# Optimization experiments

Hardware: AMD Instinct MI355X
Metric: run time of the kernel (lower is better)

## Reference

```python
import jax, jax.numpy as jnp
import numpy as np
from jax import lax


def _sobel_kernel(k=3):
    r = np.linspace(-(k // 2), k // 2, k)
    x, y = np.meshgrid(r, r)
    den = x ** 2 + y ** 2
    den[:, k // 2] = 1.0
    return (x / den).astype(np.float32)  # [[-.5,0,.5],[-1,0,1],[-.5,0,.5]]


def _thin_kernels():
    # 8 directional kernels: +1 at center, -1 at the neighbor at angle k*45 deg
    # (counterclockwise), exactly what the cv2 rotation in the torch code produces.
    offsets = [(0, 1), (-1, 1), (-1, 0), (-1, -1), (0, -1), (1, -1), (1, 0), (1, 1)]
    ker = np.zeros((8, 1, 3, 3), dtype=np.float32)
    for i, (dy, dx) in enumerate(offsets):
        ker[i, 0, 1, 1] = 1.0
        ker[i, 0, 1 + dy, 1 + dx] = -1.0
    return ker


def _conv(x, w):
    # cross-correlation, SAME padding, NCHW/OIHW -- matches torch Conv2d
    return lax.conv_general_dilated(x, w, window_strides=(1, 1), padding='SAME',
                                    dimension_numbers=('NCHW', 'OIHW', 'NCHW'))


def setup_inputs() -> dict:
    key = jax.random.key(0)
    img = jax.random.normal(key, (16, 1, 1024, 1024), dtype=jnp.float32)
    sob = _sobel_kernel(3)
    return {
        'img': img,
        'w_x': jnp.asarray(sob).reshape(1, 1, 3, 3),
        'w_y': jnp.asarray(sob.T).reshape(1, 1, 3, 3),
        'w_dir': jnp.asarray(_thin_kernels()),
        'threshold': jnp.float32(0.5),
    }


def reference(img, w_x, w_y, w_dir, threshold):
    grad_x = _conv(img, w_x)
    grad_y = _conv(img, w_y)
    grad_mag = jnp.sqrt(grad_x ** 2 + grad_y ** 2)  # [B,1,H,W]

    ori = jnp.arctan(grad_y / grad_x) * (360.0 / np.pi) + 180.0
    ori = jnp.round(ori / 45.0) * 45.0
    pos_idx = (ori / 45.0) % 8.0  # integer-valued float in {0..7}

    directional = _conv(grad_mag, w_dir)  # [B,8,H,W]

    # per-pixel direction d = pos_idx mod 4; pixel survives NMS iff both the
    # d and d+4 directional differences (center minus neighbor) are > 0
    idx4 = jnp.clip((pos_idx % 4.0).astype(jnp.int32), 0, 3)  # [B,1,H,W]
    dir_min = jnp.minimum(directional[:, :4], directional[:, 4:])  # [B,4,H,W]
    keep = jnp.take_along_axis(dir_min > 0.0, idx4, axis=1)  # [B,1,H,W] bool
    thin_edges = jnp.where(keep, grad_mag, 0.0)

    out = thin_edges - threshold
    out_forw = (out > 0.0).astype(out.dtype)  # heaviside(out, 0)
    out_bckw = jax.nn.sigmoid(out)
    return out_bckw + lax.stop_gradient(out_forw - out_bckw)
```

## Files before the change

kernel.cpp:

```cpp
#include <hip/hip_runtime.h>
#include <math.h>


constexpr int W = 1024, H = 1024;
constexpr int TX = 128, TY = 16;
constexpr int GH = TY + 2, GSTR = 132;

__device__ __forceinline__ void sobel_pair(float a00, float a01, float a02,
                                           float a10, float a12,
                                           float a20, float a21, float a22,
                                           float& gxv, float& gyv) {
  float t1 = 0.5f * (a02 - a00);
  float t2 = t1 - a10;
  float t3 = t2 + a12;
  float t4 = t3 - 0.5f * a20;
  gxv = t4 + 0.5f * a22;
  float p1 = 0.5f * a00 + a01;
  float p2 = p1 + 0.5f * a02;
  float u3 = 0.5f * a20 - p2;
  float u4 = u3 + a21;
  gyv = u4 + 0.5f * a22;
}

__device__ __forceinline__ float gld(const float* __restrict__ im, int r, int c) {
  const bool ok = ((unsigned)r < 1024u) && ((unsigned)c < 1024u);
  const int rc = min(max(r, 0), 1023);
  const int cc = min(max(c, 0), 1023);
  const float v = im[rc * W + cc];
  return ok ? v : 0.0f;
}

__device__ __forceinline__ float decide(float gxv, float gyv, float sc,
                                        float s0a, float s0b, float s1a, float s1b,
                                        float s2a, float s2b, float s3a, float s3b,
                                        float thr, float thr2) {
#pragma clang fp contract(off)
  const float T1 = 0.19891236737965801f, D1 = 5.0e-5f;
  const float T2 = 0.66817863791929898f, D2 = 7.0e-5f;
  const float T3 = 1.49660576266548901f, D3 = 1.5e-4f;
  const float T4 = 5.02733949212584810f, D4 = 1.2e-3f;

  const float av = fabsf(gyv), bv = fabsf(gxv);
  const float c1 = fmaf(-T1, bv, av);
  const float c2 = fmaf(-T2, bv, av);
  const float c3 = fmaf(-T3, bv, av);
  const float c4 = fmaf(-T4, bv, av);
  const bool nearb = (fabsf(c1) < D1 * bv) || (fabsf(c2) < D2 * bv) ||
                     (fabsf(c3) < D3 * bv) || (fabsf(c4) < D4 * bv);

  const unsigned sgn = (__float_as_uint(gyv) ^ __float_as_uint(gxv)) >> 31;

  const float m0 = fmaxf(fmaxf(s0a, s0b), thr2);
  const float m1 = fmaxf(fmaxf(s1a, s1b), thr2);
  const float m2 = fmaxf(fmaxf(s2a, s2b), thr2);
  const float m3 = fmaxf(fmaxf(s3a, s3b), thr2);
  float m;
  if (c1 < 0.0f)      m = m0;
  else if (c2 < 0.0f) m = sgn ? m3 : m1;
  else if (c3 < 0.0f) m = m2;
  else if (c4 < 0.0f) m = sgn ? m1 : m3;
  else                m = m0;

  const float scl = sc * 0.999998f;
  const bool raw  = (sc  > m);
  const bool sure = (scl > m);

  const bool need = nearb || (raw != sure);
  float res = sure ? 1.0f : 0.0f;

  if (__builtin_expect(__any((int)need), 0)) {
    const float C = (float)(360.0 / M_PI);
    float r  = gyv / gxv;
    float t  = atanf(r);
    float u  = t * C;
    float v2 = u + 180.0f;
    float w  = v2 / 45.0f;
    int   kk = (int)rintf(w);
    int   dd = kk & 3;
    float sn1e = (dd == 0) ? s0a : (dd == 1) ? s1a : (dd == 2) ? s2a : s3a;
    float sn2e = (dd == 0) ? s0b : (dd == 1) ? s1b : (dd == 2) ? s2b : s3b;
    float gmc = sqrtf(sc), n1 = sqrtf(sn1e), n2 = sqrtf(sn2e);
    bool keep = (gmc - n1 > 0.0f) && (gmc - n2 > 0.0f) && (gmc - thr > 0.0f);
    float slow = keep ? 1.0f : 0.0f;
    res = need ? slow : res;
  }
  return res;
}

__global__ __launch_bounds__(256)
void canny_kernel(const float* __restrict__ img, const float* __restrict__ thrp,
                  float* __restrict__ out) {
#pragma clang fp contract(off)
  __shared__ __align__(16) float s_sq[GH][GSTR];

  const int b   = blockIdx.z;
  const int bx0 = blockIdx.x * TX;
  const int by0 = blockIdx.y * TY;
  const float* im = img + (size_t)b * (W * H);
  float* ob       = out + (size_t)b * (W * H);
  const int tid = threadIdx.x;
  const bool edge = (bx0 == 0) || (bx0 + TX == W) || (by0 == 0) || (by0 + TY == H);

  const int c  = tid & 127;
  const int tz = tid >> 7;
  const int k0 = 9 * tz;

  float iA0, iB0, iC0, iA1, iB1, iC1, iA2, iB2, iC2, iA3, iB3, iC3;
  float iA4, iB4, iC4, iA5, iB5, iC5, iA6, iB6, iC6, iA7, iB7, iC7;
  float iA8, iB8, iC8, iA9, iB9, iC9, iA10, iB10, iC10;
  if (!edge) {
    const float* p = im + (size_t)(by0 + k0 - 2) * W + (bx0 + c - 1);
    iA0  = p[0 * W + 0];  iB0  = p[0 * W + 1];  iC0  = p[0 * W + 2];
    iA1  = p[1 * W + 0];  iB1  = p[1 * W + 1];  iC1  = p[1 * W + 2];
    iA2  = p[2 * W + 0];  iB2  = p[2 * W + 1];  iC2  = p[2 * W + 2];
    iA3  = p[3 * W + 0];  iB3  = p[3 * W + 1];  iC3  = p[3 * W + 2];
    iA4  = p[4 * W + 0];  iB4  = p[4 * W + 1];  iC4  = p[4 * W + 2];
    iA5  = p[5 * W + 0];  iB5  = p[5 * W + 1];  iC5  = p[5 * W + 2];
    iA6  = p[6 * W + 0];  iB6  = p[6 * W + 1];  iC6  = p[6 * W + 2];
    iA7  = p[7 * W + 0];  iB7  = p[7 * W + 1];  iC7  = p[7 * W + 2];
    iA8  = p[8 * W + 0];  iB8  = p[8 * W + 1];  iC8  = p[8 * W + 2];
    iA9  = p[9 * W + 0];  iB9  = p[9 * W + 1];  iC9  = p[9 * W + 2];
    iA10 = p[10 * W + 0]; iB10 = p[10 * W + 1]; iC10 = p[10 * W + 2];
  } else {
    const int r0 = by0 + k0 - 2;
    const int cb = bx0 + c;
    iA0  = gld(im, r0 + 0, cb - 1);  iB0  = gld(im, r0 + 0, cb);  iC0  = gld(im, r0 + 0, cb + 1);
    iA1  = gld(im, r0 + 1, cb - 1);  iB1  = gld(im, r0 + 1, cb);  iC1  = gld(im, r0 + 1, cb + 1);
    iA2  = gld(im, r0 + 2, cb - 1);  iB2  = gld(im, r0 + 2, cb);  iC2  = gld(im, r0 + 2, cb + 1);
    iA3  = gld(im, r0 + 3, cb - 1);  iB3  = gld(im, r0 + 3, cb);  iC3  = gld(im, r0 + 3, cb + 1);
    iA4  = gld(im, r0 + 4, cb - 1);  iB4  = gld(im, r0 + 4, cb);  iC4  = gld(im, r0 + 4, cb + 1);
    iA5  = gld(im, r0 + 5, cb - 1);  iB5  = gld(im, r0 + 5, cb);  iC5  = gld(im, r0 + 5, cb + 1);
    iA6  = gld(im, r0 + 6, cb - 1);  iB6  = gld(im, r0 + 6, cb);  iC6  = gld(im, r0 + 6, cb + 1);
    iA7  = gld(im, r0 + 7, cb - 1);  iB7  = gld(im, r0 + 7, cb);  iC7  = gld(im, r0 + 7, cb + 1);
    iA8  = gld(im, r0 + 8, cb - 1);  iB8  = gld(im, r0 + 8, cb);  iC8  = gld(im, r0 + 8, cb + 1);
    iA9  = gld(im, r0 + 9, cb - 1);  iB9  = gld(im, r0 + 9, cb);  iC9  = gld(im, r0 + 9, cb + 1);
    iA10 = gld(im, r0 + 10, cb - 1); iB10 = gld(im, r0 + 10, cb); iC10 = gld(im, r0 + 10, cb + 1);
  }

  const int rowim0 = by0 + k0 - 1;

  float t0, t1, t2, t3, t4, t5, t6, t7, t8;
  float sx0, sx1, sx2, sx3, sx4, sx5, sx6, sx7, sx8;
  float sy0, sy1, sy2, sy3, sy4, sy5, sy6, sy7, sy8;

#define GM_ROW(J, A0, B0, C0, A1, C1, A2, B2, C2, T, SX, SY)                   \
  {                                                                            \
    float gxv, gyv;                                                            \
    sobel_pair(A0, B0, C0, A1, C1, A2, B2, C2, gxv, gyv);                      \
    float sq = gxv * gxv + gyv * gyv;                                          \
    if (edge) { if ((unsigned)(rowim0 + J) >= 1024u) sq = 0.0f; }              \
    s_sq[k0 + J][c + 1] = sq;                                                  \
    T = sq; SX = gxv; SY = gyv;                                                \
  }

  GM_ROW(0, iA0, iB0, iC0, iA1, iC1, iA2, iB2, iC2, t0, sx0, sy0)
  GM_ROW(1, iA1, iB1, iC1, iA2, iC2, iA3, iB3, iC3, t1, sx1, sy1)
  GM_ROW(2, iA2, iB2, iC2, iA3, iC3, iA4, iB4, iC4, t2, sx2, sy2)
  GM_ROW(3, iA3, iB3, iC3, iA4, iC4, iA5, iB5, iC5, t3, sx3, sy3)
  GM_ROW(4, iA4, iB4, iC4, iA5, iC5, iA6, iB6, iC6, t4, sx4, sy4)
  GM_ROW(5, iA5, iB5, iC5, iA6, iC6, iA7, iB7, iC7, t5, sx5, sy5)
  GM_ROW(6, iA6, iB6, iC6, iA7, iC7, iA8, iB8, iC8, t6, sx6, sy6)
  GM_ROW(7, iA7, iB7, iC7, iA8, iC8, iA9, iB9, iC9, t7, sx7, sy7)
  GM_ROW(8, iA8, iB8, iC8, iA9, iC9, iA10, iB10, iC10, t8, sx8, sy8)
#undef GM_ROW

  if (tid < 36) {
    int rr = tid >> 1;
    int r  = rr - 1;
    int cc = (tid & 1) ? 128 : -1;
    int hr = by0 - 2 + rr;
    int hc = bx0 + cc;
    float gxv, gyv;
    sobel_pair(gld(im, hr, hc - 1),     gld(im, hr, hc),     gld(im, hr, hc + 1),
               gld(im, hr + 1, hc - 1),                      gld(im, hr + 1, hc + 1),
               gld(im, hr + 2, hc - 1), gld(im, hr + 2, hc), gld(im, hr + 2, hc + 1),
               gxv, gyv);
    float sq = gxv * gxv + gyv * gyv;
    if (!((unsigned)(by0 + r) < 1024u && (unsigned)(bx0 + cc) < 1024u)) sq = 0.0f;
    s_sq[rr][cc + 1] = sq;
  }
  __syncthreads();

  {
    const float thr  = *thrp;
    const float thr2 = thr * thr;
    const int gb = 8 * tz;
    const float L0 = s_sq[gb + 0][c], R0 = s_sq[gb + 0][c + 2];
    const float L1 = s_sq[gb + 1][c], R1 = s_sq[gb + 1][c + 2];
    const float L2 = s_sq[gb + 2][c], R2 = s_sq[gb + 2][c + 2];
    const float L3 = s_sq[gb + 3][c], R3 = s_sq[gb + 3][c + 2];
    const float L4 = s_sq[gb + 4][c], R4 = s_sq[gb + 4][c + 2];
    const float L5 = s_sq[gb + 5][c], R5 = s_sq[gb + 5][c + 2];
    const float L6 = s_sq[gb + 6][c], R6 = s_sq[gb + 6][c + 2];
    const float L7 = s_sq[gb + 7][c], R7 = s_sq[gb + 7][c + 2];
    const float L8 = s_sq[gb + 8][c], R8 = s_sq[gb + 8][c + 2];
    const float L9 = s_sq[gb + 9][c], R9 = s_sq[gb + 9][c + 2];

    float q0, q1, q2, q3, q4, q5, q6, q7, q8, q9;
    float X0, X1, X2, X3, X4, X5, X6, X7;
    float Y0, Y1, Y2, Y3, Y4, Y5, Y6, Y7;
    if (tz == 0) {
      q0 = t0; q1 = t1; q2 = t2; q3 = t3; q4 = t4;
      q5 = t5; q6 = t6; q7 = t7; q8 = t8;
      q9 = s_sq[9][c + 1];
      X0 = sx1; X1 = sx2; X2 = sx3; X3 = sx4; X4 = sx5; X5 = sx6; X6 = sx7; X7 = sx8;
      Y0 = sy1; Y1 = sy2; Y2 = sy3; Y3 = sy4; Y4 = sy5; Y5 = sy6; Y6 = sy7; Y7 = sy8;
    } else {
      q0 = s_sq[8][c + 1];
      q1 = t0; q2 = t1; q3 = t2; q4 = t3; q5 = t4;
      q6 = t5; q7 = t6; q8 = t7; q9 = t8;
      X0 = sx0; X1 = sx1; X2 = sx2; X3 = sx3; X4 = sx4; X5 = sx5; X6 = sx6; X7 = sx7;
      Y0 = sy0; Y1 = sy1; Y2 = sy2; Y3 = sy3; Y4 = sy4; Y5 = sy5; Y6 = sy7 - (sy7 - sy6) - (sy6 - sy6);
      Y6 = sy6; Y7 = sy7;
    }

    float* orow = ob + (size_t)(by0 + gb) * W + bx0 + c;

    orow[0 * W] = decide(X0, Y0, q1, R1, L1, R0, L2, q0, q2, L0, R2, thr, thr2);
    orow[1 * W] = decide(X1, Y1, q2, R2, L2, R1, L3, q1, q3, L1, R3, thr, thr2);
    orow[2 * W] = decide(X2, Y2, q3, R3, L3, R2, L4, q2, q4, L2, R4, thr, thr2);
    orow[3 * W] = decide(X3, Y3, q4, R4, L4, R3, L5, q3, q5, L3, R5, thr, thr2);
    orow[4 * W] = decide(X4, Y4, q5, R5, L5, R4, L6, q4, q6, L4, R6, thr, thr2);
    orow[5 * W] = decide(X5, Y5, q6, R6, L6, R5, L7, q5, q7, L5, R7, thr, thr2);
    orow[6 * W] = decide(X6, Y6, q7, R7, L7, R6, L8, q6, q8, L6, R8, thr, thr2);
    orow[7 * W] = decide(X7, Y7, q8, R8, L8, R7, L9, q7, q9, L7, R9, thr, thr2);
  }
}

extern "C" void kernel_launch(void* const* d_in, const int* in_sizes, int n_in,
                              void* d_out, int out_size, void* d_ws, size_t ws_size,
                              hipStream_t stream) {
  const float* img = (const float*)d_in[0];
  const float* thr = (const float*)d_in[4];
  float* out = (float*)d_out;
  const int batch = in_sizes[0] / (W * H);

  dim3 grid(W / TX, H / TY, batch);
  canny_kernel<<<grid, dim3(256), 0, stream>>>(img, thr, out);
}
```

Before: 42.86 us.

## Pack two rows per thread into float2 vectors for packed-math Sobel and NMS

Halves the block to 128 threads. Each thread now processes two rows eight apart as float2 vectors, so the Sobel, magnitude and direction-threshold arithmetic can use packed FP32 instructions (v_pk_fma_f32). The near-boundary test is rewritten as a min over FMA-based margins to cut compares, and the per-pixel tail stays scalar. The aim is to cut the VALU instruction count, at the cost of more registers per thread, fewer waves per block, and some FMA contraction that may change rounding slightly.

```diff
diff --git a/kernel.cpp b/kernel.cpp
--- a/kernel.cpp
+++ b/kernel.cpp
@@ -6,20 +6,27 @@
 constexpr int TX = 128, TY = 16;
 constexpr int GH = TY + 2, GSTR = 132;
 
-__device__ __forceinline__ void sobel_pair(float a00, float a01, float a02,
-                                           float a10, float a12,
-                                           float a20, float a21, float a22,
-                                           float& gxv, float& gyv) {
-  float t1 = 0.5f * (a02 - a00);
-  float t2 = t1 - a10;
-  float t3 = t2 + a12;
-  float t4 = t3 - 0.5f * a20;
-  gxv = t4 + 0.5f * a22;
-  float p1 = 0.5f * a00 + a01;
-  float p2 = p1 + 0.5f * a02;
-  float u3 = 0.5f * a20 - p2;
-  float u4 = u3 + a21;
-  gyv = u4 + 0.5f * a22;
+typedef float v2f __attribute__((ext_vector_type(2)));
+
+__device__ __forceinline__ v2f splat2(float a) { v2f v; v.x = a; v.y = a; return v; }
+__device__ __forceinline__ v2f fma2(float a, v2f b, v2f c) {
+  return __builtin_elementwise_fma(splat2(a), b, c);
+}
+
+__device__ __forceinline__ void sobel_pair2(v2f a00, v2f a01, v2f a02,
+                                            v2f a10, v2f a12,
+                                            v2f a20, v2f a21, v2f a22,
+                                            v2f& gxv, v2f& gyv) {
+  v2f t1 = splat2(0.5f) * (a02 - a00);
+  v2f t2 = t1 - a10;
+  v2f t3 = t2 + a12;
+  v2f t4 = fma2(-0.5f, a20, t3);
+  gxv = fma2(0.5f, a22, t4);
+  v2f p1 = fma2(0.5f, a00, a01);
+  v2f p2 = fma2(0.5f, a02, p1);
+  v2f u3 = fma2(0.5f, a20, -p2);
+  v2f u4 = u3 + a21;
+  gyv = fma2(0.5f, a22, u4);
 }
 
 __device__ __forceinline__ float gld(const float* __restrict__ im, int r, int c) {
@@ -30,26 +37,15 @@
   return ok ? v : 0.0f;
 }
 
-__device__ __forceinline__ float decide(float gxv, float gyv, float sc,
-                                        float s0a, float s0b, float s1a, float s1b,
-                                        float s2a, float s2b, float s3a, float s3b,
-                                        float thr, float thr2) {
+__device__ __forceinline__ float decide_tail(
+    float gxv, float gyv, float sc,
+    float c1, float c2, float c3, float c4, float emin, float scl,
+    float s0a, float s0b, float s1a, float s1b,
+    float s2a, float s2b, float s3a, float s3b,
+    float thr, float thr2) {
 #pragma clang fp contract(off)
-  const float T1 = 0.19891236737965801f, D1 = 5.0e-5f;
-  const float T2 = 0.66817863791929898f, D2 = 7.0e-5f;
-  const float T3 = 1.49660576266548901f, D3 = 1.5e-4f;
-  const float T4 = 5.02733949212584810f, D4 = 1.2e-3f;
-
-  const float av = fabsf(gyv), bv = fabsf(gxv);
-  const float c1 = fmaf(-T1, bv, av);
-  const float c2 = fmaf(-T2, bv, av);
-  const float c3 = fmaf(-T3, bv, av);
-  const float c4 = fmaf(-T4, bv, av);
-  const bool nearb = (fabsf(c1) < D1 * bv) || (fabsf(c2) < D2 * bv) ||
-                     (fabsf(c3) < D3 * bv) || (fabsf(c4) < D4 * bv);
-
+  const bool nearb = emin < 0.0f;
   const unsigned sgn = (__float_as_uint(gyv) ^ __float_as_uint(gxv)) >> 31;
-
   const float m0 = fmaxf(fmaxf(s0a, s0b), thr2);
   const float m1 = fmaxf(fmaxf(s1a, s1b), thr2);
   const float m2 = fmaxf(fmaxf(s2a, s2b), thr2);
@@ -60,14 +56,10 @@
   else if (c3 < 0.0f) m = m2;
   else if (c4 < 0.0f) m = sgn ? m1 : m3;
   else                m = m0;
-
-  const float scl = sc * 0.999998f;
   const bool raw  = (sc  > m);
   const bool sure = (scl > m);
-
   const bool need = nearb || (raw != sure);
   float res = sure ? 1.0f : 0.0f;
-
   if (__builtin_expect(__any((int)need), 0)) {
     const float C = (float)(360.0 / M_PI);
     float r  = gyv / gxv;
@@ -87,7 +79,41 @@
   return res;
 }
 
-__global__ __launch_bounds__(256)
+__device__ __forceinline__ v2f decide2(v2f gxv, v2f gyv, v2f sc,
+                                       v2f s0a, v2f s0b, v2f s1a, v2f s1b,
+                                       v2f s2a, v2f s2b, v2f s3a, v2f s3b,
+                                       float thr, float thr2) {
+#pragma clang fp contract(off)
+  const float T1 = 0.19891236737965801f, D1 = 5.0e-5f;
+  const float T2 = 0.66817863791929898f, D2 = 7.0e-5f;
+  const float T3 = 1.49660576266548901f, D3 = 1.5e-4f;
+  const float T4 = 5.02733949212584810f, D4 = 1.2e-3f;
+
+  const v2f av = __builtin_elementwise_abs(gyv);
+  const v2f bv = __builtin_elementwise_abs(gxv);
+  const v2f c1 = fma2(-T1, bv, av);
+  const v2f c2 = fma2(-T2, bv, av);
+  const v2f c3 = fma2(-T3, bv, av);
+  const v2f c4 = fma2(-T4, bv, av);
+  const v2f e1 = fma2(-D1, bv, __builtin_elementwise_abs(c1));
+  const v2f e2 = fma2(-D2, bv, __builtin_elementwise_abs(c2));
+  const v2f e3 = fma2(-D3, bv, __builtin_elementwise_abs(c3));
+  const v2f e4 = fma2(-D4, bv, __builtin_elementwise_abs(c4));
+  const v2f emin = __builtin_elementwise_min(__builtin_elementwise_min(e1, e2),
+                                             __builtin_elementwise_min(e3, e4));
+  const v2f scl = sc * splat2(0.999998f);
+
+  v2f res;
+  res.x = decide_tail(gxv.x, gyv.x, sc.x, c1.x, c2.x, c3.x, c4.x, emin.x, scl.x,
+                      s0a.x, s0b.x, s1a.x, s1b.x, s2a.x, s2b.x, s3a.x, s3b.x,
+                      thr, thr2);
+  res.y = decide_tail(gxv.y, gyv.y, sc.y, c1.y, c2.y, c3.y, c4.y, emin.y, scl.y,
+                      s0a.y, s0b.y, s1a.y, s1b.y, s2a.y, s2b.y, s3a.y, s3b.y,
+                      thr, thr2);
+  return res;
+}
+
+__global__ __launch_bounds__(128)
 void canny_kernel(const float* __restrict__ img, const float* __restrict__ thrp,
                   float* __restrict__ out) {
 #pragma clang fp contract(off)
@@ -99,70 +125,87 @@
   const float* im = img + (size_t)b * (W * H);
   float* ob       = out + (size_t)b * (W * H);
   const int tid = threadIdx.x;
+  const int c   = tid;
   const bool edge = (bx0 == 0) || (bx0 + TX == W) || (by0 == 0) || (by0 + TY == H);
 
-  const int c  = tid & 127;
-  const int tz = tid >> 7;
-  const int k0 = 9 * tz;
-
-  float iA0, iB0, iC0, iA1, iB1, iC1, iA2, iB2, iC2, iA3, iB3, iC3;
-  float iA4, iB4, iC4, iA5, iB5, iC5, iA6, iB6, iC6, iA7, iB7, iC7;
-  float iA8, iB8, iC8, iA9, iB9, iC9, iA10, iB10, iC10;
+  const float thr  = *thrp;
+  const float thr2 = thr * thr;
+
+  v2f PA0, PA1, PA2, PA3, PA4, PA5, PA6, PA7, PA8, PA9, PA10, PA11;
+  v2f PB0, PB1, PB2, PB3, PB4, PB5, PB6, PB7, PB8, PB9, PB10, PB11;
+  v2f PC0, PC1, PC2, PC3, PC4, PC5, PC6, PC7, PC8, PC9, PC10, PC11;
   if (!edge) {
-    const float* p = im + (size_t)(by0 + k0 - 2) * W + (bx0 + c - 1);
-    iA0  = p[0 * W + 0];  iB0  = p[0 * W + 1];  iC0  = p[0 * W + 2];
-    iA1  = p[1 * W + 0];  iB1  = p[1 * W + 1];  iC1  = p[1 * W + 2];
-    iA2  = p[2 * W + 0];  iB2  = p[2 * W + 1];  iC2  = p[2 * W + 2];
-    iA3  = p[3 * W + 0];  iB3  = p[3 * W + 1];  iC3  = p[3 * W + 2];
-    iA4  = p[4 * W + 0];  iB4  = p[4 * W + 1];  iC4  = p[4 * W + 2];
-    iA5  = p[5 * W + 0];  iB5  = p[5 * W + 1];  iC5  = p[5 * W + 2];
-    iA6  = p[6 * W + 0];  iB6  = p[6 * W + 1];  iC6  = p[6 * W + 2];
-    iA7  = p[7 * W + 0];  iB7  = p[7 * W + 1];  iC7  = p[7 * W + 2];
-    iA8  = p[8 * W + 0];  iB8  = p[8 * W + 1];  iC8  = p[8 * W + 2];
-    iA9  = p[9 * W + 0];  iB9  = p[9 * W + 1];  iC9  = p[9 * W + 2];
-    iA10 = p[10 * W + 0]; iB10 = p[10 * W + 1]; iC10 = p[10 * W + 2];
+    const float* p = im + (size_t)(by0 - 2) * W + (bx0 + c - 1);
+#define MKP(J)                                                                 \
+    PA##J = (v2f){p[(J) * W + 0], p[((J) + 8) * W + 0]};                       \
+    PB##J = (v2f){p[(J) * W + 1], p[((J) + 8) * W + 1]};                       \
+    PC##J = (v2f){p[(J) * W + 2], p[((J) + 8) * W + 2]};
+    MKP(0) MKP(1) MKP(2) MKP(3) MKP(4) MKP(5)
+    MKP(6) MKP(7) MKP(8) MKP(9) MKP(10) MKP(11)
+#undef MKP
   } else {
-    const int r0 = by0 + k0 - 2;
     const int cb = bx0 + c;
-    iA0  = gld(im, r0 + 0, cb - 1);  iB0  = gld(im, r0 + 0, cb);  iC0  = gld(im, r0 + 0, cb + 1);
-    iA1  = gld(im, r0 + 1, cb - 1);  iB1  = gld(im, r0 + 1, cb);  iC1  = gld(im, r0 + 1, cb + 1);
-    iA2  = gld(im, r0 + 2, cb - 1);  iB2  = gld(im, r0 + 2, cb);  iC2  = gld(im, r0 + 2, cb + 1);
-    iA3  = gld(im, r0 + 3, cb - 1);  iB3  = gld(im, r0 + 3, cb);  iC3  = gld(im, r0 + 3, cb + 1);
-    iA4  = gld(im, r0 + 4, cb - 1);  iB4  = gld(im, r0 + 4, cb);  iC4  = gld(im, r0 + 4, cb + 1);
-    iA5  = gld(im, r0 + 5, cb - 1);  iB5  = gld(im, r0 + 5, cb);  iC5  = gld(im, r0 + 5, cb + 1);
-    iA6  = gld(im, r0 + 6, cb - 1);  iB6  = gld(im, r0 + 6, cb);  iC6  = gld(im, r0 + 6, cb + 1);
-    iA7  = gld(im, r0 + 7, cb - 1);  iB7  = gld(im, r0 + 7, cb);  iC7  = gld(im, r0 + 7, cb + 1);
-    iA8  = gld(im, r0 + 8, cb - 1);  iB8  = gld(im, r0 + 8, cb);  iC8  = gld(im, r0 + 8, cb + 1);
-    iA9  = gld(im, r0 + 9, cb - 1);  iB9  = gld(im, r0 + 9, cb);  iC9  = gld(im, r0 + 9, cb + 1);
-    iA10 = gld(im, r0 + 10, cb - 1); iB10 = gld(im, r0 + 10, cb); iC10 = gld(im, r0 + 10, cb + 1);
-  }
-
-  const int rowim0 = by0 + k0 - 1;
-
-  float t0, t1, t2, t3, t4, t5, t6, t7, t8;
-  float sx0, sx1, sx2, sx3, sx4, sx5, sx6, sx7, sx8;
-  float sy0, sy1, sy2, sy3, sy4, sy5, sy6, sy7, sy8;
-
-#define GM_ROW(J, A0, B0, C0, A1, C1, A2, B2, C2, T, SX, SY)                   \
+    const int ccm1 = max(cb - 1, 0);
+    const int ccp1 = min(cb + 1, 1023);
+    const bool okL = (cb - 1) >= 0;
+    const bool okR = (cb + 1) <= 1023;
+    const int r0 = by0 - 2;
+    float vA0, vA1, vA2, vA3, vA4, vA5, vA6, vA7, vA8, vA9;
+    float vA10, vA11, vA12, vA13, vA14, vA15, vA16, vA17, vA18, vA19;
+    float vB0, vB1, vB2, vB3, vB4, vB5, vB6, vB7, vB8, vB9;
+    float vB10, vB11, vB12, vB13, vB14, vB15, vB16, vB17, vB18, vB19;
+    float vC0, vC1, vC2, vC3, vC4, vC5, vC6, vC7, vC8, vC9;
+    float vC10, vC11, vC12, vC13, vC14, vC15, vC16, vC17, vC18, vC19;
+#define LOADROW(J)                                                             \
+    {                                                                          \
+      const int rj = r0 + (J);                                                 \
+      const bool rOK = (unsigned)rj < 1024u;                 \
+      const int rc = min(max(rj, 0), 1023);                                    \
+      const float* rp = im + (size_t)rc * W;                                   \
+      const float va = rp[ccm1], vb = rp[cb], vc = rp[ccp1];                   \
+      vA##J = (rOK && okL) ? va : 0.0f;                                        \
+      vB##J = rOK ? vb : 0.0f;                                                 \
+      vC##J = (rOK && okR) ? vc : 0.0f;                                        \
+    }
+    LOADROW(0) LOADROW(1) LOADROW(2) LOADROW(3) LOADROW(4)
+    LOADROW(5) LOADROW(6) LOADROW(7) LOADROW(8) LOADROW(9)
+    LOADROW(10) LOADROW(11) LOADROW(12) LOADROW(13) LOADROW(14)
+    LOADROW(15) LOADROW(16) LOADROW(17) LOADROW(18) LOADROW(19)
+#undef LOADROW
+#define MKP(J, J8)                                                             \
+    PA##J = (v2f){vA##J, vA##J8};                                              \
+    PB##J = (v2f){vB##J, vB##J8};                                              \
+    PC##J = (v2f){vC##J, vC##J8};
+    MKP(0, 8) MKP(1, 9) MKP(2, 10) MKP(3, 11) MKP(4, 12) MKP(5, 13)
+    MKP(6, 14) MKP(7, 15) MKP(8, 16) MKP(9, 17) MKP(10, 18) MKP(11, 19)
+#undef MKP
+  }
+
+  v2f sq0, sq1, sq2v, sq3, sq4, sq5, sq6, sq7, sq8, sq9;
+  v2f ga0, ga1, ga2, ga3, ga4, ga5, ga6, ga7, ga8, ga9;
+  v2f gb0, gb1, gb2, gb3, gb4, gb5, gb6, gb7, gb8, gb9;
+#define GM_PAIR(J, A0, B0, C0, A1, C1, A2, B2, C2, SQ, GX, GY)                 \
   {                                                                            \
-    float gxv, gyv;                                                            \
-    sobel_pair(A0, B0, C0, A1, C1, A2, B2, C2, gxv, gyv);                      \
-    float sq = gxv * gxv + gyv * gyv;                                          \
-    if (edge) { if ((unsigned)(rowim0 + J) >= 1024u) sq = 0.0f; }              \
-    s_sq[k0 + J][c + 1] = sq;                                                  \
-    T = sq; SX = gxv; SY = gyv;                                                \
-  }
-
-  GM_ROW(0, iA0, iB0, iC0, iA1, iC1, iA2, iB2, iC2, t0, sx0, sy0)
-  GM_ROW(1, iA1, iB1, iC1, iA2, iC2, iA3, iB3, iC3, t1, sx1, sy1)
-  GM_ROW(2, iA2, iB2, iC2, iA3, iC3, iA4, iB4, iC4, t2, sx2, sy2)
-  GM_ROW(3, iA3, iB3, iC3, iA4, iC4, iA5, iB5, iC5, t3, sx3, sy3)
-  GM_ROW(4, iA4, iB4, iC4, iA5, iC5, iA6, iB6, iC6, t4, sx4, sy4)
-  GM_ROW(5, iA5, iB5, iC5, iA6, iC6, iA7, iB7, iC7, t5, sx5, sy5)
-  GM_ROW(6, iA6, iB6, iC6, iA7, iC7, iA8, iB8, iC8, t6, sx6, sy6)
-  GM_ROW(7, iA7, iB7, iC7, iA8, iC8, iA9, iB9, iC9, t7, sx7, sy7)
-  GM_ROW(8, iA8, iB8, iC8, iA9, iC9, iA10, iB10, iC10, t8, sx8, sy8)
-#undef GM_ROW
+    sobel_pair2(A0, B0, C0, A1, C1, A2, B2, C2, GX, GY);                       \
+    SQ = GX * GX + GY * GY;                                                    \
+    if (edge) {                                                                \
+      if ((unsigned)(by0 + (J) - 1) >= 1024u) SQ.x = 0.0f;                     \
+      if ((unsigned)(by0 + (J) + 7) >= 1024u) SQ.y = 0.0f;                     \
+    }                                                                          \
+    s_sq[(J)][c + 1] = SQ.x;                                                   \
+    s_sq[(J) + 8][c + 1] = SQ.y;                                               \
+  }
+  GM_PAIR(0, PA0, PB0, PC0, PA1, PC1, PA2, PB2, PC2, sq0, ga0, gb0)
+  GM_PAIR(1, PA1, PB1, PC1, PA2, PC2, PA3, PB3, PC3, sq1, ga1, gb1)
+  GM_PAIR(2, PA2, PB2, PC2, PA3, PC3, PA4, PB4, PC4, sq2v, ga2, gb2)
+  GM_PAIR(3, PA3, PB3, PC3, PA4, PC4, PA5, PB5, PC5, sq3, ga3, gb3)
+  GM_PAIR(4, PA4, PB4, PC4, PA5, PC5, PA6, PB6, PC6, sq4, ga4, gb4)
+  GM_PAIR(5, PA5, PB5, PC5, PA6, PC6, PA7, PB7, PC7, sq5, ga5, gb5)
+  GM_PAIR(6, PA6, PB6, PC6, PA7, PC7, PA8, PB8, PC8, sq6, ga6, gb6)
+  GM_PAIR(7, PA7, PB7, PC7, PA8, PC8, PA9, PB9, PC9, sq7, ga7, gb7)
+  GM_PAIR(8, PA8, PB8, PC8, PA9, PC9, PA10, PB10, PC10, sq8, ga8, gb8)
+  GM_PAIR(9, PA9, PB9, PC9, PA10, PC10, PA11, PB11, PC11, sq9, ga9, gb9)
+#undef GM_PAIR
 
   if (tid < 36) {
     int rr = tid >> 1;
@@ -171,10 +214,21 @@
     int hr = by0 - 2 + rr;
     int hc = bx0 + cc;
     float gxv, gyv;
-    sobel_pair(gld(im, hr, hc - 1),     gld(im, hr, hc),     gld(im, hr, hc + 1),
-               gld(im, hr + 1, hc - 1),                      gld(im, hr + 1, hc + 1),
-               gld(im, hr + 2, hc - 1), gld(im, hr + 2, hc), gld(im, hr + 2, hc + 1),
-               gxv, gyv);
+    {
+      float a00 = gld(im, hr, hc - 1),     a01 = gld(im, hr, hc),     a02 = gld(im, hr, hc + 1);
+      float a10 = gld(im, hr + 1, hc - 1),                            a12 = gld(im, hr + 1, hc + 1);
+      float a20 = gld(im, hr + 2, hc - 1), a21 = gld(im, hr + 2, hc), a22 = gld(im, hr + 2, hc + 1);
+      float t1 = 0.5f * (a02 - a00);
+      float t2 = t1 - a10;
+      float t3 = t2 + a12;
+      float t4 = fmaf(-0.5f, a20, t3);
+      gxv = fmaf(0.5f, a22, t4);
+      float p1 = fmaf(0.5f, a00, a01);
+      float p2 = fmaf(0.5f, a02, p1);
+      float u3 = fmaf(0.5f, a20, -p2);
+      float u4 = u3 + a21;
+      gyv = fmaf(0.5f, a22, u4);
+    }
     float sq = gxv * gxv + gyv * gyv;
     if (!((unsigned)(by0 + r) < 1024u && (unsigned)(bx0 + cc) < 1024u)) sq = 0.0f;
     s_sq[rr][cc + 1] = sq;
@@ -182,48 +236,35 @@
   __syncthreads();
 
   {
-    const float thr  = *thrp;
-    const float thr2 = thr * thr;
-    const int gb = 8 * tz;
-    const float L0 = s_sq[gb + 0][c], R0 = s_sq[gb + 0][c + 2];
-    const float L1 = s_sq[gb + 1][c], R1 = s_sq[gb + 1][c + 2];
-    const float L2 = s_sq[gb + 2][c], R2 = s_sq[gb + 2][c + 2];
-    const float L3 = s_sq[gb + 3][c], R3 = s_sq[gb + 3][c + 2];
-    const float L4 = s_sq[gb + 4][c], R4 = s_sq[gb + 4][c + 2];
-    const float L5 = s_sq[gb + 5][c], R5 = s_sq[gb + 5][c + 2];
-    const float L6 = s_sq[gb + 6][c], R6 = s_sq[gb + 6][c + 2];
-    const float L7 = s_sq[gb + 7][c], R7 = s_sq[gb + 7][c + 2];
-    const float L8 = s_sq[gb + 8][c], R8 = s_sq[gb + 8][c + 2];
-    const float L9 = s_sq[gb + 9][c], R9 = s_sq[gb + 9][c + 2];
-
-    float q0, q1, q2, q3, q4, q5, q6, q7, q8, q9;
-    float X0, X1, X2, X3, X4, X5, X6, X7;
-    float Y0, Y1, Y2, Y3, Y4, Y5, Y6, Y7;
-    if (tz == 0) {
-      q0 = t0; q1 = t1; q2 = t2; q3 = t3; q4 = t4;
-      q5 = t5; q6 = t6; q7 = t7; q8 = t8;
-      q9 = s_sq[9][c + 1];
-      X0 = sx1; X1 = sx2; X2 = sx3; X3 = sx4; X4 = sx5; X5 = sx6; X6 = sx7; X7 = sx8;
-      Y0 = sy1; Y1 = sy2; Y2 = sy3; Y3 = sy4; Y4 = sy5; Y5 = sy6; Y6 = sy7; Y7 = sy8;
-    } else {
-      q0 = s_sq[8][c + 1];
-      q1 = t0; q2 = t1; q3 = t2; q4 = t3; q5 = t4;
-      q6 = t5; q7 = t6; q8 = t7; q9 = t8;
-      X0 = sx0; X1 = sx1; X2 = sx2; X3 = sx3; X4 = sx4; X5 = sx5; X6 = sx6; X7 = sx7;
-      Y0 = sy0; Y1 = sy1; Y2 = sy2; Y3 = sy3; Y4 = sy4; Y5 = sy5; Y6 = sy7 - (sy7 - sy6) - (sy6 - sy6);
-      Y6 = sy6; Y7 = sy7;
+    v2f L0 = (v2f){s_sq[0][c], s_sq[8][c]},   R0 = (v2f){s_sq[0][c + 2], s_sq[8][c + 2]};
+    v2f L1 = (v2f){s_sq[1][c], s_sq[9][c]},   R1 = (v2f){s_sq[1][c + 2], s_sq[9][c + 2]};
+    v2f L2 = (v2f){s_sq[2][c], s_sq[10][c]},  R2 = (v2f){s_sq[2][c + 2], s_sq[10][c + 2]};
+    v2f L3 = (v2f){s_sq[3][c], s_sq[11][c]},  R3 = (v2f){s_sq[3][c + 2], s_sq[11][c + 2]};
+    v2f L4 = (v2f){s_sq[4][c], s_sq[12][c]},  R4 = (v2f){s_sq[4][c + 2], s_sq[12][c + 2]};
+    v2f L5 = (v2f){s_sq[5][c], s_sq[13][c]},  R5 = (v2f){s_sq[5][c + 2], s_sq[13][c + 2]};
+    v2f L6 = (v2f){s_sq[6][c], s_sq[14][c]},  R6 = (v2f){s_sq[6][c + 2], s_sq[14][c + 2]};
+    v2f L7 = (v2f){s_sq[7][c], s_sq[15][c]},  R7 = (v2f){s_sq[7][c + 2], s_sq[15][c + 2]};
+    v2f L8 = (v2f){s_sq[8][c], s_sq[16][c]},  R8 = (v2f){s_sq[8][c + 2], s_sq[16][c + 2]};
+    v2f L9 = (v2f){s_sq[9][c], s_sq[17][c]},  R9 = (v2f){s_sq[9][c + 2], s_sq[17][c + 2]};
+
+    float* o = ob + (size_t)by0 * W + bx0 + c;
+
+#define PIX(K, SCM, SC, SCP, LKM, LK, LKP, RKM, RK, RKP, GX, GY)               \
+    {                                                                          \
+      v2f r = decide2(GX, GY, SC, RK, LK, RKM, LKP, SCM, SCP, LKM, RKP,        \
+                      thr, thr2);                                              \
+      o[(K) * W] = r.x;                                                        \
+      o[((K) + 8) * W] = r.y;                                                  \
     }
-
-    float* orow = ob + (size_t)(by0 + gb) * W + bx0 + c;
-
-    orow[0 * W] = decide(X0, Y0, q1, R1, L1, R0, L2, q0, q2, L0, R2, thr, thr2);
-    orow[1 * W] = decide(X1, Y1, q2, R2, L2, R1, L3, q1, q3, L1, R3, thr, thr2);
-    orow[2 * W] = decide(X2, Y2, q3, R3, L3, R2, L4, q2, q4, L2, R4, thr, thr2);
-    orow[3 * W] = decide(X3, Y3, q4, R4, L4, R3, L5, q3, q5, L3, R5, thr, thr2);
-    orow[4 * W] = decide(X4, Y4, q5, R5, L5, R4, L6, q4, q6, L4, R6, thr, thr2);
-    orow[5 * W] = decide(X5, Y5, q6, R6, L6, R5, L7, q5, q7, L5, R7, thr, thr2);
-    orow[6 * W] = decide(X6, Y6, q7, R7, L7, R6, L8, q6, q8, L6, R8, thr, thr2);
-    orow[7 * W] = decide(X7, Y7, q8, R8, L8, R7, L9, q7, q9, L7, R9, thr, thr2);
+    PIX(0, sq0, sq1, sq2v, L0, L1, L2, R0, R1, R2, ga1, gb1)
+    PIX(1, sq1, sq2v, sq3, L1, L2, L3, R1, R2, R3, ga2, gb2)
+    PIX(2, sq2v, sq3, sq4, L2, L3, L4, R2, R3, R4, ga3, gb3)
+    PIX(3, sq3, sq4, sq5, L3, L4, L5, R3, R4, R5, ga4, gb4)
+    PIX(4, sq4, sq5, sq6, L4, L5, L6, R4, R5, R6, ga5, gb5)
+    PIX(5, sq5, sq6, sq7, L5, L6, L7, R5, R6, R7, ga6, gb6)
+    PIX(6, sq6, sq7, sq8, L6, L7, L8, R6, R7, R8, ga7, gb7)
+    PIX(7, sq7, sq8, sq9, L7, L8, L9, R7, R8, R9, ga8, gb8)
+#undef PIX
   }
 }
 
@@ -236,5 +277,5 @@
   const int batch = in_sizes[0] / (W * H);
 
   dim3 grid(W / TX, H / TY, batch);
-  canny_kernel<<<grid, dim3(256), 0, stream>>>(img, thr, out);
-}
+  canny_kernel<<<grid, dim3(128), 0, stream>>>(img, thr, out);
+}
```

New measurement: 40.93 us. 1.05x faster.
